# Kernel optimization log

Hardware: AMD Instinct MI355X
Metric: run time of the kernel (lower is better)

Reference implementation:

```python
import jax, jax.numpy as jnp
import numpy as np

EMBED_DIM = 2048
NUM_HEADS = 16
HEAD_DIM = EMBED_DIM // NUM_HEADS
BATCH, SEQ = 4, 4096


def setup_inputs() -> dict:
    key = jax.random.key(0)
    k1, k2, k3, k4 = jax.random.split(key, 4)
    scale = 1.0 / np.sqrt(EMBED_DIM)
    x = jax.random.normal(k1, (BATCH, SEQ, EMBED_DIM), dtype=jnp.float32)
    W_qkv = jax.random.normal(k2, (EMBED_DIM, 3 * EMBED_DIM), dtype=jnp.float32) * scale
    W_out = jax.random.normal(k3, (EMBED_DIM, EMBED_DIM), dtype=jnp.float32) * scale
    b_out = jax.random.normal(k4, (EMBED_DIM,), dtype=jnp.float32) * 0.01
    return {"x": x, "W_qkv": W_qkv, "W_out": W_out, "b_out": b_out}


def reference(x, W_qkv, W_out, b_out):
    b, s, _ = x.shape
    # qkv: (b, s, 3, h, d)
    qkv = (x @ W_qkv).reshape(b, s, 3, NUM_HEADS, HEAD_DIM)
    q, k, v = qkv[:, :, 0], qkv[:, :, 1], qkv[:, :, 2]
    # NOTE: faithful to source — scores mix HEADS per token: (b, s, h, h)
    scores = jnp.einsum('bshd,bsHd->bshH', q, k) / jnp.sqrt(jnp.float32(HEAD_DIM))
    w = jax.nn.softmax(scores, axis=-1)
    attn = jnp.einsum('bshH,bsHd->bshd', w, v).reshape(b, s, EMBED_DIM)
    return attn @ W_out + b_out
```

## Files before the change

kernel.cpp:

```cpp
#include <hip/hip_runtime.h>
#include <hip/hip_bf16.h>
#include <cstdint>


#define TOKENS 16384
#define EMB    2048
#define NQKV   6144

typedef __bf16 bf16x8_t __attribute__((ext_vector_type(8)));
typedef float  f32x4_t  __attribute__((ext_vector_type(4)));

#define GLOAD16(gsrc, ldst)                                                    \
  __builtin_amdgcn_global_load_lds(                                            \
      (const __attribute__((address_space(1))) void*)(uintptr_t)(gsrc),        \
      (__attribute__((address_space(3))) void*)(uint32_t)(uintptr_t)(ldst),    \
      16, 0, 0)

static __device__ __forceinline__ unsigned short f32_to_bf16_bits(float f) {
  union { float f; uint32_t u; } x; x.f = f;
  uint32_t u = x.u;
  u += 0x7fffu + ((u >> 16) & 1u);
  return (unsigned short)(u >> 16);
}

__global__ __launch_bounds__(256) void cvt_f32_bf16(
    const float4* __restrict__ in, ushort4* __restrict__ out, int n4) {
  const int stride = gridDim.x * blockDim.x;
  for (int i = blockIdx.x * blockDim.x + threadIdx.x; i < n4; i += stride) {
    float4 v = in[i];
    ushort4 o;
    o.x = f32_to_bf16_bits(v.x);
    o.y = f32_to_bf16_bits(v.y);
    o.z = f32_to_bf16_bits(v.z);
    o.w = f32_to_bf16_bits(v.w);
    out[i] = o;
  }
}

__global__ __launch_bounds__(256) void transpose_cvt(
    const float* __restrict__ in, unsigned short* __restrict__ out, int R, int C) {
  __shared__ float tile[32][33];
  const int bx = blockIdx.x * 32;
  const int by = blockIdx.y * 32;
  const int tx = threadIdx.x;
  const int ty = threadIdx.y;
#pragma unroll
  for (int j = 0; j < 32; j += 8)
    tile[ty + j][tx] = in[(size_t)(by + ty + j) * C + bx + tx];
  __syncthreads();
#pragma unroll
  for (int j = 0; j < 32; j += 8)
    out[(size_t)(bx + ty + j) * R + by + tx] = f32_to_bf16_bits(tile[tx][ty + j]);
}

template <bool OUT_BF16>
__global__ __launch_bounds__(512, 1) void gemm_bt(
    const unsigned short* __restrict__ A,
    const unsigned short* __restrict__ BT,
    unsigned short* __restrict__ Cb,
    float* __restrict__ Cf,
    const float* __restrict__ bias,
    int M, int N) {
  constexpr int K = 2048;
  constexpr int BK = 64;
  constexpr int NKT = K / BK;
  __shared__ __align__(16) char lds[131072];

  const int nbx = N / 256;
  const int nwg = gridDim.x;
  const int bid = blockIdx.x;
  const int swzb = (bid & 7) * (nwg >> 3) + (bid >> 3);
  const int by = swzb / nbx;
  const int bx = swzb % nbx;

  const int t    = threadIdx.x;
  const int lane = t & 63;
  const int wid  = t >> 6;
  const int wr   = wid >> 2;
  const int wc   = wid & 3;
  const int lr   = lane & 15;
  const int g    = lane >> 4;

  const unsigned short* aSrc = A  + (size_t)by * 256 * K;
  const unsigned short* bSrc = BT + (size_t)bx * 256 * K;

  int aoff[2], boff[2];
#pragma unroll
  for (int i = 0; i < 2; ++i) {
    const int p   = (i * 512 + t) * 16;
    const int lo  = p ^ (((p >> 7) & 7) << 4);
    const int rih = lo >> 7;
    const int kbe = (lo & 127) >> 1;
    aoff[i] = (((rih >> 6) << 7) + (rih & 63)) * K + kbe;
    boff[i] = (((rih >> 5) << 6) + (rih & 31)) * K + kbe;
  }
  const int ldst = wid << 10;

  auto stageA = [&](int h, int k0, char* bufA) {
#pragma unroll
    for (int i = 0; i < 2; ++i)
      GLOAD16(aSrc + aoff[i] + h * (64 * K) + k0, bufA + h * 16384 + i * 8192 + ldst);
  };
  auto stageB = [&](int h, int k0, char* bufB) {
#pragma unroll
    for (int i = 0; i < 2; ++i)
      GLOAD16(bSrc + boff[i] + h * (32 * K) + k0, bufB + h * 16384 + i * 8192 + ldst);
  };

  const int sw   = (lr & 7) << 4;
  const int col0 = (g * 16) ^ sw;
  const int col1 = (64 + g * 16) ^ sw;
  const int aRow = (wr * 64 + lr) * 128;
  const int bRow = (wc * 32 + lr) * 128;

  f32x4_t acc[8][4] = {};
  bf16x8_t av0[4][2], av1[4][2];
  bf16x8_t bv0[2][2], bv1[2][2];

#define LDA_INTO(dst, bufA_, q)                                                \
  {                                                                            \
    const char* _b = (bufA_) + (q) * 16384 + aRow;                             \
    _Pragma("unroll") for (int m2 = 0; m2 < 4; ++m2) {                         \
      dst[m2][0] = *(const bf16x8_t*)(_b + m2 * 2048 + col0);                  \
      dst[m2][1] = *(const bf16x8_t*)(_b + m2 * 2048 + col1);                  \
    }                                                                          \
  }
#define LDB_INTO(dst, bufB_, pair)                                             \
  {                                                                            \
    _Pragma("unroll") for (int e = 0; e < 2; ++e) {                            \
      const int nf = (pair) * 2 + e;                                           \
      const char* _b = (bufB_) + (nf >> 1) * 16384 + (nf & 1) * 2048 + bRow;   \
      dst[e][0] = *(const bf16x8_t*)(_b + col0);                               \
      dst[e][1] = *(const bf16x8_t*)(_b + col1);                               \
    }                                                                          \
  }
#define MFMAQ(AV, BV, Q, PAIR)                                                 \
  _Pragma("unroll") for (int m2 = 0; m2 < 4; ++m2)                             \
  _Pragma("unroll") for (int e = 0; e < 2; ++e)                                \
  _Pragma("unroll") for (int ks = 0; ks < 2; ++ks)                             \
    acc[(Q) * 4 + m2][(PAIR) * 2 + e] = __builtin_amdgcn_mfma_f32_16x16x32_bf16( \
        AV[m2][ks], BV[e][ks], acc[(Q) * 4 + m2][(PAIR) * 2 + e], 0, 0, 0);

#define SBR __builtin_amdgcn_sched_barrier(0)

#define BODY(KT, S1, S2, VMN)                                                  \
  {                                                                            \
    char* cA = lds + ((KT) & 1) * 65536;                                       \
    char* cB = cA + 32768;                                                     \
    char* nA = lds + (((KT) + 1) & 1) * 65536;                                 \
    const int k1 = ((KT) + 1) * BK, k2 = ((KT) + 2) * BK;                      \
                  \
    LDA_INTO(av0, cA, 0);                                                      \
    LDB_INTO(bv0, cB, 0);                                                      \
    LDB_INTO(bv1, cB, 1);                                                      \
    LDA_INTO(av1, cA, 1); SBR;                                                 \
    if (S1) { stageA(1, k1, nA); } SBR;                                        \
    asm volatile("s_waitcnt lgkmcnt(0)" ::: "memory"); SBR;                    \
    __builtin_amdgcn_s_setprio(1);                                             \
    MFMAQ(av0, bv0, 0, 0);                                                     \
    MFMAQ(av0, bv1, 0, 1);                                                     \
    __builtin_amdgcn_s_setprio(0); SBR;                                        \
    __builtin_amdgcn_s_barrier();                                              \
      \
    if (S2) { stageB(0, k2, cB); stageB(1, k2, cB); stageA(0, k2, cA); } SBR;  \
    __builtin_amdgcn_s_setprio(1);                                             \
    MFMAQ(av1, bv1, 1, 1);                                                     \
    MFMAQ(av1, bv0, 1, 0);                                                     \
    __builtin_amdgcn_s_setprio(0); SBR;                                        \
    asm volatile("s_waitcnt vmcnt(" #VMN ")" ::: "memory"); SBR;               \
    __builtin_amdgcn_s_barrier();                                              \
  }

  {
    char* b0A = lds;
    char* b0B = lds + 32768;
    char* b1A = lds + 65536;
    char* b1B = b1A + 32768;
    stageA(0, 0, b0A); stageA(1, 0, b0A);
    stageB(0, 0, b0B); stageB(1, 0, b0B);
    stageB(0, BK, b1B); stageB(1, BK, b1B);
    stageA(0, BK, b1A);
    asm volatile("s_waitcnt vmcnt(6)" ::: "memory");
    __builtin_amdgcn_s_barrier();
  }

  for (int kt = 0; kt < NKT - 2; ++kt) {
    BODY(kt, 1, 1, 6);
  }
  BODY(NKT - 2, 1, 0, 0);
  BODY(NKT - 1, 0, 0, 0);

  const int rbase = by * 256 + wr * 128 + g * 4;
  const int cbase = bx * 256 + wc * 64 + lr;
#pragma unroll
  for (int m = 0; m < 8; ++m) {
#pragma unroll
    for (int nf = 0; nf < 4; ++nf) {
      const int col = cbase + nf * 16;
#pragma unroll
      for (int j = 0; j < 4; ++j) {
        const size_t off = (size_t)(rbase + (m >> 2) * 64 + (m & 3) * 16 + j) * N + col;
        if constexpr (OUT_BF16) {
          Cb[off] = f32_to_bf16_bits(acc[m][nf][j]);
        } else {
          Cf[off] = acc[m][nf][j] + bias[col];
        }
      }
    }
  }
#undef LDA_INTO
#undef LDB_INTO
#undef MFMAQ
#undef SBR
#undef BODY
}

__global__ __launch_bounds__(256) void attn_heads(
    const unsigned short* __restrict__ qkv,
    unsigned short* __restrict__ attn) {
  __shared__ __align__(16) unsigned short sQKV[NQKV];
  __shared__ float sW[16][16];

  const int t = threadIdx.x;
  const size_t qbase = (size_t)blockIdx.x * NQKV;

  const uint4* gp = (const uint4*)(qkv + qbase);
  uint4* l = (uint4*)sQKV;
#pragma unroll
  for (int i = 0; i < 3; ++i) {
    const int idx = i * 256 + t;
    int dst = idx;
    if (idx >= 256 && idx < 512) {
      const int r = (idx - 256) >> 4;
      const int c = idx & 15;
      dst = 256 + r * 16 + (c ^ (r & 7));
    }
    l[dst] = gp[idx];
  }
  __syncthreads();

  const int h = t >> 4;
  const int H = t & 15;
  const bf16x8_t* q8 = (const bf16x8_t*)sQKV + h * 16;
  const bf16x8_t* k8 = (const bf16x8_t*)sQKV + 256;
  float s = 0.f;
#pragma unroll
  for (int d8 = 0; d8 < 16; ++d8) {
    bf16x8_t qv = q8[d8];
    bf16x8_t kv = k8[H * 16 + (d8 ^ (H & 7))];
#pragma unroll
    for (int j = 0; j < 8; ++j)
      s = fmaf((float)qv[j], (float)kv[j], s);
  }
  s *= 0.08838834764831843f;

  float mx = s;
#pragma unroll
  for (int o = 8; o; o >>= 1) mx = fmaxf(mx, __shfl_xor(mx, o));
  const float e = __expf(s - mx);
  float sum = e;
#pragma unroll
  for (int o = 8; o; o >>= 1) sum += __shfl_xor(sum, o);
  sW[h][H] = e / sum;
  __syncthreads();

  const int d0c = t & 15;
  const bf16x8_t* v8 = (const bf16x8_t*)sQKV + 512;
  float accv[8] = {};
#pragma unroll
  for (int j = 0; j < 16; ++j) {
    const float w = sW[h][j];
    const bf16x8_t vv = v8[j * 16 + d0c];
#pragma unroll
    for (int jj = 0; jj < 8; ++jj)
      accv[jj] = fmaf(w, (float)vv[jj], accv[jj]);
  }
  bf16x8_t o;
#pragma unroll
  for (int jj = 0; jj < 8; ++jj) o[jj] = (__bf16)accv[jj];
  *(bf16x8_t*)(attn + (size_t)blockIdx.x * EMB + h * 128 + d0c * 8) = o;
}

extern "C" void kernel_launch(void* const* d_in, const int* in_sizes, int n_in,
                              void* d_out, int out_size, void* d_ws, size_t ws_size,
                              hipStream_t stream) {
  const float* x    = (const float*)d_in[0];
  const float* Wqkv = (const float*)d_in[1];
  const float* Wout = (const float*)d_in[2];
  const float* bout = (const float*)d_in[3];
  float* out = (float*)d_out;

  unsigned short* xb    = (unsigned short*)d_ws;
  unsigned short* wqkvT = xb    + (size_t)33554432;
  unsigned short* woutT = wqkvT + (size_t)12582912;
  unsigned short* qkv   = woutT + (size_t)4194304;
  unsigned short* attn  = qkv   + (size_t)100663296;

  cvt_f32_bf16<<<2048, 256, 0, stream>>>((const float4*)x, (ushort4*)xb, 33554432 / 4);
  transpose_cvt<<<dim3(6144 / 32, 2048 / 32), dim3(32, 8), 0, stream>>>(Wqkv, wqkvT, 2048, 6144);
  transpose_cvt<<<dim3(2048 / 32, 2048 / 32), dim3(32, 8), 0, stream>>>(Wout, woutT, 2048, 2048);
  gemm_bt<true><<<(16384 / 256) * (6144 / 256), 512, 0, stream>>>(
      xb, wqkvT, qkv, nullptr, nullptr, 16384, 6144);
  attn_heads<<<TOKENS, 256, 0, stream>>>(qkv, attn);
  gemm_bt<false><<<(16384 / 256) * (2048 / 256), 512, 0, stream>>>(
      attn, woutT, nullptr, out, bout, 16384, 2048);
}
```

Measured before the change: 616.5 us.

## Switch GEMM to 32x32x16 MFMA with lane-linear LDS layout

Replaces the 16x16x32 bf16 MFMA tiling with 32x32x16 MFMA tiles and reorganises the LDS staging so each lane's fragment is contiguous (row per lane, k-chunk per group), removing the XOR swizzle. All A/B fragments for the K-step are read at once before the MFMA batches, and the epilogue is remapped to the 32x32 accumulator layout. The aim is fewer MFMA issues and LDS reads per FLOP. The unswizzled lane-linear layout trades the swizzle for simpler addressing and may add register pressure from holding all fragments.

New measurement: 725.8 us. +17.7%, slower.

```diff
diff --git a/kernel.cpp b/kernel.cpp
--- a/kernel.cpp
+++ b/kernel.cpp
@@ -7,8 +7,8 @@
 #define EMB    2048
 #define NQKV   6144
 
-typedef __bf16 bf16x8_t __attribute__((ext_vector_type(8)));
-typedef float  f32x4_t  __attribute__((ext_vector_type(4)));
+typedef __bf16 bf16x8_t  __attribute__((ext_vector_type(8)));
+typedef float  f32x16_t  __attribute__((ext_vector_type(16)));
 
 #define GLOAD16(gsrc, ldst)                                                    \
   __builtin_amdgcn_global_load_lds(                                            \
@@ -78,68 +78,52 @@
   const int wid  = t >> 6;
   const int wr   = wid >> 2;
   const int wc   = wid & 3;
-  const int lr   = lane & 15;
-  const int g    = lane >> 4;
+  const int r31  = lane & 31;
+  const int kg   = lane >> 5;
 
   const unsigned short* aSrc = A  + (size_t)by * 256 * K;
   const unsigned short* bSrc = BT + (size_t)bx * 256 * K;
 
-  int aoff[2], boff[2];
-#pragma unroll
-  for (int i = 0; i < 2; ++i) {
-    const int p   = (i * 512 + t) * 16;
-    const int lo  = p ^ (((p >> 7) & 7) << 4);
-    const int rih = lo >> 7;
-    const int kbe = (lo & 127) >> 1;
-    aoff[i] = (((rih >> 6) << 7) + (rih & 63)) * K + kbe;
-    boff[i] = (((rih >> 5) << 6) + (rih & 31)) * K + kbe;
-  }
-  const int ldst = wid << 10;
+  int offs[2], loff[2];
+#pragma unroll
+  for (int j = 0; j < 2; ++j) {
+    const int idx = wid * 2 + j;
+    loff[j] = idx * 1024;
+    offs[j] = ((idx >> 2) * 32 + r31) * K + (idx & 3) * 16 + kg * 8;
+  }
 
   auto stageA = [&](int h, int k0, char* bufA) {
 #pragma unroll
-    for (int i = 0; i < 2; ++i)
-      GLOAD16(aSrc + aoff[i] + h * (64 * K) + k0, bufA + h * 16384 + i * 8192 + ldst);
+    for (int j = 0; j < 2; ++j)
+      GLOAD16(aSrc + offs[j] + h * (128 * K) + k0, bufA + h * 16384 + loff[j]);
   };
   auto stageB = [&](int h, int k0, char* bufB) {
 #pragma unroll
-    for (int i = 0; i < 2; ++i)
-      GLOAD16(bSrc + boff[i] + h * (32 * K) + k0, bufB + h * 16384 + i * 8192 + ldst);
+    for (int j = 0; j < 2; ++j)
+      GLOAD16(bSrc + offs[j] + h * (128 * K) + k0, bufB + h * 16384 + loff[j]);
   };
 
-  const int sw   = (lr & 7) << 4;
-  const int col0 = (g * 16) ^ sw;
-  const int col1 = (64 + g * 16) ^ sw;
-  const int aRow = (wr * 64 + lr) * 128;
-  const int bRow = (wc * 32 + lr) * 128;
-
-  f32x4_t acc[8][4] = {};
-  bf16x8_t av0[4][2], av1[4][2];
-  bf16x8_t bv0[2][2], bv1[2][2];
-
-#define LDA_INTO(dst, bufA_, q)                                                \
-  {                                                                            \
-    const char* _b = (bufA_) + (q) * 16384 + aRow;                             \
-    _Pragma("unroll") for (int m2 = 0; m2 < 4; ++m2) {                         \
-      dst[m2][0] = *(const bf16x8_t*)(_b + m2 * 2048 + col0);                  \
-      dst[m2][1] = *(const bf16x8_t*)(_b + m2 * 2048 + col1);                  \
-    }                                                                          \
-  }
-#define LDB_INTO(dst, bufB_, pair)                                             \
-  {                                                                            \
-    _Pragma("unroll") for (int e = 0; e < 2; ++e) {                            \
-      const int nf = (pair) * 2 + e;                                           \
-      const char* _b = (bufB_) + (nf >> 1) * 16384 + (nf & 1) * 2048 + bRow;   \
-      dst[e][0] = *(const bf16x8_t*)(_b + col0);                               \
-      dst[e][1] = *(const bf16x8_t*)(_b + col1);                               \
-    }                                                                          \
-  }
-#define MFMAQ(AV, BV, Q, PAIR)                                                 \
-  _Pragma("unroll") for (int m2 = 0; m2 < 4; ++m2)                             \
-  _Pragma("unroll") for (int e = 0; e < 2; ++e)                                \
-  _Pragma("unroll") for (int ks = 0; ks < 2; ++ks)                             \
-    acc[(Q) * 4 + m2][(PAIR) * 2 + e] = __builtin_amdgcn_mfma_f32_16x16x32_bf16( \
-        AV[m2][ks], BV[e][ks], acc[(Q) * 4 + m2][(PAIR) * 2 + e], 0, 0, 0);
+  const int aBase = wr * 16384 + lane * 16;
+  const int bBase = wc * 8192 + lane * 16;
+
+  f32x16_t acc[4][2] = {};
+  bf16x8_t av[4][4];
+  bf16x8_t bv[2][4];
+
+#define RD_ALL(cA_, cB_)                                                       \
+  _Pragma("unroll") for (int mf = 0; mf < 4; ++mf)                             \
+  _Pragma("unroll") for (int ks = 0; ks < 4; ++ks)                             \
+    av[mf][ks] = *(const bf16x8_t*)((cA_) + aBase + mf * 4096 + ks * 1024);    \
+  _Pragma("unroll") for (int nf = 0; nf < 2; ++nf)                             \
+  _Pragma("unroll") for (int ks = 0; ks < 4; ++ks)                             \
+    bv[nf][ks] = *(const bf16x8_t*)((cB_) + bBase + nf * 4096 + ks * 1024);
+
+#define MFMAH(MF0)                                                             \
+  _Pragma("unroll") for (int mf = (MF0); mf < (MF0) + 2; ++mf)                 \
+  _Pragma("unroll") for (int nf = 0; nf < 2; ++nf)                             \
+  _Pragma("unroll") for (int ks = 0; ks < 4; ++ks)                             \
+    acc[mf][nf] = __builtin_amdgcn_mfma_f32_32x32x16_bf16(                     \
+        av[mf][ks], bv[nf][ks], acc[mf][nf], 0, 0, 0);
 
 #define SBR __builtin_amdgcn_sched_barrier(0)
 
@@ -149,23 +133,18 @@
     char* cB = cA + 32768;                                                     \
     char* nA = lds + (((KT) + 1) & 1) * 65536;                                 \
     const int k1 = ((KT) + 1) * BK, k2 = ((KT) + 2) * BK;                      \
-                  \
-    LDA_INTO(av0, cA, 0);                                                      \
-    LDB_INTO(bv0, cB, 0);                                                      \
-    LDB_INTO(bv1, cB, 1);                                                      \
-    LDA_INTO(av1, cA, 1); SBR;                                                 \
+                                                        \
+    RD_ALL(cA, cB); SBR;                                                       \
     if (S1) { stageA(1, k1, nA); } SBR;                                        \
     asm volatile("s_waitcnt lgkmcnt(0)" ::: "memory"); SBR;                    \
     __builtin_amdgcn_s_setprio(1);                                             \
-    MFMAQ(av0, bv0, 0, 0);                                                     \
-    MFMAQ(av0, bv1, 0, 1);                                                     \
+    MFMAH(0);                                                                  \
     __builtin_amdgcn_s_setprio(0); SBR;                                        \
     __builtin_amdgcn_s_barrier();                                              \
-      \
+           \
     if (S2) { stageB(0, k2, cB); stageB(1, k2, cB); stageA(0, k2, cA); } SBR;  \
     __builtin_amdgcn_s_setprio(1);                                             \
-    MFMAQ(av1, bv1, 1, 1);                                                     \
-    MFMAQ(av1, bv0, 1, 0);                                                     \
+    MFMAH(2);                                                                  \
     __builtin_amdgcn_s_setprio(0); SBR;                                        \
     asm volatile("s_waitcnt vmcnt(" #VMN ")" ::: "memory"); SBR;               \
     __builtin_amdgcn_s_barrier();                                              \
@@ -190,27 +169,27 @@
   BODY(NKT - 2, 1, 0, 0);
   BODY(NKT - 1, 0, 0, 0);
 
-  const int rbase = by * 256 + wr * 128 + g * 4;
-  const int cbase = bx * 256 + wc * 64 + lr;
-#pragma unroll
-  for (int m = 0; m < 8; ++m) {
-#pragma unroll
-    for (int nf = 0; nf < 4; ++nf) {
-      const int col = cbase + nf * 16;
-#pragma unroll
-      for (int j = 0; j < 4; ++j) {
-        const size_t off = (size_t)(rbase + (m >> 2) * 64 + (m & 3) * 16 + j) * N + col;
+  const int rbase = by * 256 + wr * 128 + 4 * kg;
+  const int cbase = bx * 256 + wc * 64 + r31;
+#pragma unroll
+  for (int mf = 0; mf < 4; ++mf) {
+#pragma unroll
+    for (int nf = 0; nf < 2; ++nf) {
+      const int col = cbase + nf * 32;
+#pragma unroll
+      for (int reg = 0; reg < 16; ++reg) {
+        const int row = rbase + mf * 32 + (reg & 3) + 8 * (reg >> 2);
+        const size_t off = (size_t)row * N + col;
         if constexpr (OUT_BF16) {
-          Cb[off] = f32_to_bf16_bits(acc[m][nf][j]);
+          Cb[off] = f32_to_bf16_bits(acc[mf][nf][reg]);
         } else {
-          Cf[off] = acc[m][nf][j] + bias[col];
+          Cf[off] = acc[mf][nf][reg] + bias[col];
         }
       }
     }
   }
-#undef LDA_INTO
-#undef LDB_INTO
-#undef MFMAQ
+#undef RD_ALL
+#undef MFMAH
 #undef SBR
 #undef BODY
 }
```

## Restructure GEMM main loop into four-phase interleaved LDS read/MFMA schedule

Applied to the files above, without the earlier changes.

Splits each K-tile iteration of the GEMM into four MFMA quadrants. Each quadrant is preceded by a single LDS fragment load and a global-to-LDS stage, and the loop is unrolled by two so the first B fragment of the next tile is prefetched into ping-pong registers. This is meant to cut register pressure (one A fragment set instead of two) and spread LDS reads and global stages across the compute so memory latency overlaps with MFMA. In exchange it adds more workgroup barriers per iteration and changes the prologue staging order, which could add sync overhead or raise hazard risk.

Measured after the change: 612.6 us. No clear change (-0.6%).

```diff
diff --git a/kernel.cpp b/kernel.cpp
--- a/kernel.cpp
+++ b/kernel.cpp
@@ -114,8 +114,9 @@
   const int bRow = (wc * 32 + lr) * 128;
 
   f32x4_t acc[8][4] = {};
-  bf16x8_t av0[4][2], av1[4][2];
-  bf16x8_t bv0[2][2], bv1[2][2];
+  bf16x8_t av[4][2];
+  bf16x8_t bvA[2][2], bvB[2][2];
+  bf16x8_t bv1[2][2];
 
 #define LDA_INTO(dst, bufA_, q)                                                \
   {                                                                            \
@@ -142,33 +143,43 @@
         AV[m2][ks], BV[e][ks], acc[(Q) * 4 + m2][(PAIR) * 2 + e], 0, 0, 0);
 
 #define SBR __builtin_amdgcn_sched_barrier(0)
-
-#define BODY(KT, S1, S2, VMN)                                                  \
+#define BARR __builtin_amdgcn_s_barrier()
+#define LGKM0 asm volatile("s_waitcnt lgkmcnt(0)" ::: "memory"); SBR;
+#define P1_ __builtin_amdgcn_s_setprio(1);
+#define P0_ __builtin_amdgcn_s_setprio(0); SBR;
+
+#define BODY(KT, BVC, BVN, S1, S2, VMN)                                        \
   {                                                                            \
     char* cA = lds + ((KT) & 1) * 65536;                                       \
     char* cB = cA + 32768;                                                     \
-    char* nA = lds + (((KT) + 1) & 1) * 65536;                                 \
+    char* nB = lds + (((KT) + 1) & 1) * 65536 + 32768;                         \
     const int k1 = ((KT) + 1) * BK, k2 = ((KT) + 2) * BK;                      \
                   \
-    LDA_INTO(av0, cA, 0);                                                      \
-    LDB_INTO(bv0, cB, 0);                                                      \
-    LDB_INTO(bv1, cB, 1);                                                      \
-    LDA_INTO(av1, cA, 1); SBR;                                                 \
-    if (S1) { stageA(1, k1, nA); } SBR;                                        \
-    asm volatile("s_waitcnt lgkmcnt(0)" ::: "memory"); SBR;                    \
-    __builtin_amdgcn_s_setprio(1);                                             \
-    MFMAQ(av0, bv0, 0, 0);                                                     \
-    MFMAQ(av0, bv1, 0, 1);                                                     \
-    __builtin_amdgcn_s_setprio(0); SBR;                                        \
-    __builtin_amdgcn_s_barrier();                                              \
-      \
-    if (S2) { stageB(0, k2, cB); stageB(1, k2, cB); stageA(0, k2, cA); } SBR;  \
-    __builtin_amdgcn_s_setprio(1);                                             \
-    MFMAQ(av1, bv1, 1, 1);                                                     \
-    MFMAQ(av1, bv0, 1, 0);                                                     \
-    __builtin_amdgcn_s_setprio(0); SBR;                                        \
+    LDA_INTO(av, cA, 0); SBR;                                                  \
+    if (S1) { stageB(0, k1, nB); } SBR;                                        \
+    BARR; LGKM0; P1_;                                                          \
+    MFMAQ(av, BVC, 0, 0);                                                      \
+    P0_; BARR;                                                                 \
+          \
+    LDB_INTO(bv1, cB, 1); SBR;                                                 \
+    if (S2) { stageA(0, k2, cA); } SBR;                                        \
+    BARR; LGKM0; P1_;                                                          \
+    MFMAQ(av, bv1, 0, 1);                                                      \
+    P0_; BARR;                                                                 \
+           \
+    LDA_INTO(av, cA, 1); SBR;                                                  \
+    if (S2) { stageB(1, k2, cB); } SBR;                                        \
+    BARR; LGKM0; P1_;                                                          \
+    MFMAQ(av, bv1, 1, 1);                                                      \
+    P0_; BARR;                                                                 \
+                     \
+    if (S2) { stageA(1, k2, cA); } SBR;                                        \
     asm volatile("s_waitcnt vmcnt(" #VMN ")" ::: "memory"); SBR;               \
-    __builtin_amdgcn_s_barrier();                                              \
+    BARR;                                                                      \
+    if (S1) { LDB_INTO(BVN, nB, 0); } SBR;                                     \
+    P1_;                                                                       \
+    MFMAQ(av, BVC, 1, 0);                                                      \
+    P0_; BARR;                                                                 \
   }
 
   {
@@ -178,17 +189,21 @@
     char* b1B = b1A + 32768;
     stageA(0, 0, b0A); stageA(1, 0, b0A);
     stageB(0, 0, b0B); stageB(1, 0, b0B);
-    stageB(0, BK, b1B); stageB(1, BK, b1B);
     stageA(0, BK, b1A);
+    stageB(1, BK, b1B);
+    stageA(1, BK, b1A);
     asm volatile("s_waitcnt vmcnt(6)" ::: "memory");
-    __builtin_amdgcn_s_barrier();
-  }
-
-  for (int kt = 0; kt < NKT - 2; ++kt) {
-    BODY(kt, 1, 1, 6);
-  }
-  BODY(NKT - 2, 1, 0, 0);
-  BODY(NKT - 1, 0, 0, 0);
+    BARR;
+    LDB_INTO(bvA, b0B, 0);
+    SBR;
+  }
+
+  for (int kt = 0; kt < NKT - 2; kt += 2) {
+    BODY(kt,     bvA, bvB, 1, 1, 6);
+    BODY(kt + 1, bvB, bvA, 1, 1, 6);
+  }
+  BODY(NKT - 2, bvA, bvB, 1, 0, 0);
+  BODY(NKT - 1, bvB, bvA, 0, 0, 0);
 
   const int rbase = by * 256 + wr * 128 + g * 4;
   const int cbase = bx * 256 + wc * 64 + lr;
@@ -212,6 +227,10 @@
 #undef LDB_INTO
 #undef MFMAQ
 #undef SBR
+#undef BARR
+#undef LGKM0
+#undef P1_
+#undef P0_
 #undef BODY
 }
 
```
